# Performance work log

Hardware: AMD Instinct MI355X
Metric: run time of the kernel (lower is better)

## Reference

```python
import jax, jax.numpy as jnp
import numpy as np

B, H, SQ, SK, D, INT, F = 1, 32, 2048, 2048, 128, 128, 32
THOLD = 0.5


def _mlp(x, W1, b1, W2, b2, W3, b3):
    # x: [b,h,s,d]; W*: [h,out,in] (torch Linear layout), y = x @ W^T + b, per head
    h = jax.nn.silu(jnp.einsum('bhsd,hid->bhsi', x, W1) + b1[None, :, None, :])
    h = jax.nn.silu(jnp.einsum('bhsi,hji->bhsj', h, W2) + b2[None, :, None, :])
    return jnp.einsum('bhsj,hfj->bhsf', h, W3) + b3[None, :, None, :]


def setup_inputs() -> dict:
    key = jax.random.key(0)
    ks = jax.random.split(key, 16)
    sc = 0.05  # small init so tanh stays in its linear-ish range
    inp = {
        'K': jax.random.normal(ks[0], (B, H, SK, D), jnp.float32),
        'Q': jax.random.normal(ks[1], (B, H, SQ, D), jnp.float32),
        'Wk1': jax.random.normal(ks[2], (H, INT, D), jnp.float32) * sc,
        'bk1': jax.random.normal(ks[3], (H, INT), jnp.float32) * sc,
        'Wk2': jax.random.normal(ks[4], (H, INT, INT), jnp.float32) * sc,
        'bk2': jax.random.normal(ks[5], (H, INT), jnp.float32) * sc,
        'Wk3': jax.random.normal(ks[6], (H, F, INT), jnp.float32) * sc,
        'bk3': jax.random.normal(ks[7], (H, F), jnp.float32) * sc,
        'Wq1': jax.random.normal(ks[8], (H, INT, D), jnp.float32) * sc,
        'bq1': jax.random.normal(ks[9], (H, INT), jnp.float32) * sc,
        'Wq2': jax.random.normal(ks[10], (H, INT, INT), jnp.float32) * sc,
        'bq2': jax.random.normal(ks[11], (H, INT), jnp.float32) * sc,
        'Wq3': jax.random.normal(ks[12], (H, F, INT), jnp.float32) * sc,
        'bq3': jax.random.normal(ks[13], (H, F), jnp.float32) * sc,
    }
    return inp


def reference(K, Q, Wk1, bk1, Wk2, bk2, Wk3, bk3, Wq1, bq1, Wq2, bq2, Wq3, bq3):
    # soft (hard=False) path of USA.forward
    Kl = jnp.tanh(_mlp(K, Wk1, bk1, Wk2, bk2, Wk3, bk3))  # [b,h,sk,F]
    Ql = jnp.tanh(_mlp(Q, Wq1, bq1, Wq2, bq2, Wq3, bq3))  # [b,h,sq,F]
    scores = jnp.einsum('bhtf,bhsf->bhts', Ql, Kl)        # [b,h,sq,sk]
    sq, sk = Q.shape[2], K.shape[2]
    causal = jnp.tril(jnp.ones((sq, sk), dtype=bool), k=sk - sq)
    mask_val = jnp.asarray(jnp.finfo(scores.dtype).min, scores.dtype)
    scores = jnp.where(causal[None, None], scores, mask_val)
    return jax.nn.sigmoid(scores - THOLD)
```

## Files before the change

### kernel.cpp

```cpp
#include <hip/hip_runtime.h>

#define NH  32
#define SEQ 2048
#define DIM 128
#define FD  32

typedef short          short8 __attribute__((ext_vector_type(8)));
typedef float          f32x4  __attribute__((ext_vector_type(4)));
typedef unsigned short u16x8  __attribute__((ext_vector_type(8)));

static __device__ __forceinline__ unsigned short f2bf(float f) {
    unsigned int u = __builtin_bit_cast(unsigned int, f);
    u += 0x7fffu + ((u >> 16) & 1u);
    return (unsigned short)(u >> 16);
}
static __device__ __forceinline__ float fexp(float x) {
    return __builtin_amdgcn_exp2f(x * 1.44269504088896f);
}
static __device__ __forceinline__ float sigm(float x) {
    return __builtin_amdgcn_rcpf(1.0f + fexp(-x));
}
static __device__ __forceinline__ float silu_f(float x) { return x * sigm(x); }
static __device__ __forceinline__ float tanh_f(float x) {
    return 1.0f - 2.0f * __builtin_amdgcn_rcpf(fexp(2.0f * x) + 1.0f);
}

#define WPH 36864
#define WPS (32 * WPH)

__global__ __launch_bounds__(256) void prep_weights(
    const float* __restrict__ Wk1, const float* __restrict__ Wk2,
    const float* __restrict__ Wk3, const float* __restrict__ Wq1,
    const float* __restrict__ Wq2, const float* __restrict__ Wq3,
    unsigned short* __restrict__ wimg) {
    int c = blockIdx.x * 256 + threadIdx.x;
    int s = (c >= 147456) ? 1 : 0;
    c -= s * 147456;
    const float* src;
    int dst;
    int sB = s * WPS;
    if (c < 65536) {
        int h = c >> 11, idx = c & 2047;
        int r = idx >> 4, jb = (idx & 15) * 8;
        src = (s ? Wq1 : Wk1) + h * 16384 + r * 128 + jb;
        dst = sB + h * WPH + r * 128 + (jb ^ ((r & 7) << 3));
    } else if (c < 131072) {
        int cc = c - 65536;
        int h = cc >> 11, idx = cc & 2047;
        int r = idx >> 4, jb = (idx & 15) * 8;
        src = (s ? Wq2 : Wk2) + h * 16384 + r * 128 + jb;
        dst = sB + h * WPH + 16384 + r * 128 + (jb ^ ((r & 7) << 3));
    } else {
        int cc = c - 131072;
        int h = cc >> 9, idx = cc & 511;
        int r = idx >> 4, jb = (idx & 15) * 8;
        src = (s ? Wq3 : Wk3) + h * 4096 + r * 128 + jb;
        dst = sB + h * WPH + 32768 + r * 128 + (jb ^ ((r & 7) << 3));
    }
    f32x4 u0 = *(const f32x4*)src;
    f32x4 u1 = *(const f32x4*)(src + 4);
    u16x8 p;
    p[0] = f2bf(u0[0]); p[1] = f2bf(u0[1]); p[2] = f2bf(u0[2]); p[3] = f2bf(u0[3]);
    p[4] = f2bf(u1[0]); p[5] = f2bf(u1[1]); p[6] = f2bf(u1[2]); p[7] = f2bf(u1[3]);
    *(u16x8*)(&wimg[dst]) = p;
}

template <int OT, int ACT>
static __device__ __forceinline__ void compute_layer(
    const short8 a[4], const unsigned short* W,
    const float* __restrict__ bias, unsigned short* dst, int lane, int wid) {
    int r0 = lane & 15, q = lane >> 4, kb = q * 8;
#pragma unroll
    for (int ot = 0; ot < OT; ++ot) {
        int wrow = ot * 16 + r0;
        int sw   = (wrow & 7) << 3;
        short8 b[4];
#pragma unroll
        for (int ks = 0; ks < 4; ++ks)
            b[ks] = *(const short8*)(&W[wrow * 128 + ((ks * 32 + kb) ^ sw)]);
        f32x4 acc = {0.f, 0.f, 0.f, 0.f};
#pragma unroll
        for (int ks = 0; ks < 4; ++ks)
            acc = __builtin_amdgcn_mfma_f32_16x16x32_bf16(a[ks], b[ks], acc, 0, 0, 0);
        float bv = bias[wrow];
#pragma unroll
        for (int r = 0; r < 4; ++r) {
            float y = acc[r] + bv;
            float v = (ACT == 0) ? silu_f(y) : tanh_f(y);
            int orow = wid * 16 + q * 4 + r;
            int ocol = ot * 16 + r0;
            dst[orow * 128 + (ocol ^ ((orow & 7) << 3))] = f2bf(v);
        }
    }
}

static __device__ __forceinline__ void compute_layer3_reg(
    const short8 a[4], const short8 w3f[2][4],
    const float* __restrict__ bias, unsigned short* dst, int lane, int wid) {
    int r0 = lane & 15, q = lane >> 4;
#pragma unroll
    for (int ot = 0; ot < 2; ++ot) {
        f32x4 acc = {0.f, 0.f, 0.f, 0.f};
#pragma unroll
        for (int ks = 0; ks < 4; ++ks)
            acc = __builtin_amdgcn_mfma_f32_16x16x32_bf16(a[ks], w3f[ot][ks], acc, 0, 0, 0);
        float bv = bias[ot * 16 + r0];
#pragma unroll
        for (int r = 0; r < 4; ++r) {
            float v = tanh_f(acc[r] + bv);
            dst[(wid * 16 + q * 4 + r) * FD + ot * 16 + r0] = f2bf(v);
        }
    }
}

__global__ __launch_bounds__(256) void mlp_kernel(
    const float* __restrict__ K,  const float* __restrict__ Q,
    const float* __restrict__ bk1, const float* __restrict__ bk2,
    const float* __restrict__ bk3, const float* __restrict__ bq1,
    const float* __restrict__ bq2, const float* __restrict__ bq3,
    const unsigned short* __restrict__ wimg,
    unsigned short* __restrict__ Kl, unsigned short* __restrict__ Ql) {
    __shared__ unsigned short wb[128 * 128];
    __shared__ unsigned short act[64 * 128];
    __shared__ unsigned short outb[64 * FD];
    int raw = blockIdx.x;
    int bid = (raw & 7) * 256 + (raw >> 3);
    int tb  = bid & 31;
    int h   = (bid >> 5) & 31;
    int s   = bid >> 10;

    const float* X  = s ? Q : K;
    const unsigned short* Wb = wimg + s * WPS + h * WPH;
    const float* B1 = (s ? bq1 : bk1) + h * 128;
    const float* B2 = (s ? bq2 : bk2) + h * 128;
    const float* B3 = (s ? bq3 : bk3) + h * FD;
    unsigned short* gout = (s ? Ql : Kl) + ((size_t)h * SEQ + (size_t)tb * 64) * FD;

    int tid = threadIdx.x, lane = tid & 63, wid = tid >> 6;
    int r0 = lane & 15, kb = (lane >> 4) * 8;

    short8 w3f[2][4];
    {
        const unsigned short* W3g = Wb + 32768;
        int sw = (r0 & 7) << 3;
#pragma unroll
        for (int ot = 0; ot < 2; ++ot)
#pragma unroll
            for (int ks = 0; ks < 4; ++ks)
                w3f[ot][ks] = *(const short8*)(&W3g[(ot * 16 + r0) * 128 + ((ks * 32 + kb) ^ sw)]);
    }

    const u16x8* wsrc = (const u16x8*)Wb;
#pragma unroll
    for (int i = 0; i < 8; ++i)
        *(u16x8*)(&wb[(i * 256 + tid) * 8]) = wsrc[i * 256 + tid];

    short8 a[4];
    const float* xs = X + ((size_t)h * SEQ + (size_t)tb * 64) * DIM;
    int row = wid * 16 + r0;
#pragma unroll
    for (int ks = 0; ks < 4; ++ks) {
        const float* p = xs + row * 128 + ks * 32 + kb;
        f32x4 u0 = *(const f32x4*)p;
        f32x4 u1 = *(const f32x4*)(p + 4);
        short8 t;
        t[0] = f2bf(u0[0]); t[1] = f2bf(u0[1]); t[2] = f2bf(u0[2]); t[3] = f2bf(u0[3]);
        t[4] = f2bf(u1[0]); t[5] = f2bf(u1[1]); t[6] = f2bf(u1[2]); t[7] = f2bf(u1[3]);
        a[ks] = t;
    }
    __syncthreads();
    compute_layer<8, 0>(a, wb, B1, act, lane, wid);
    __syncthreads();
#pragma unroll
    for (int i = 0; i < 8; ++i)
        *(u16x8*)(&wb[(i * 256 + tid) * 8]) = wsrc[2048 + i * 256 + tid];
    __syncthreads();
    {
        int sw = (row & 7) << 3;
#pragma unroll
        for (int ks = 0; ks < 4; ++ks)
            a[ks] = *(const short8*)(&act[row * 128 + ((ks * 32 + kb) ^ sw)]);
    }
    compute_layer<8, 0>(a, wb, B2, act, lane, wid);
    {
        int sw = (row & 7) << 3;
#pragma unroll
        for (int ks = 0; ks < 4; ++ks)
            a[ks] = *(const short8*)(&act[row * 128 + ((ks * 32 + kb) ^ sw)]);
    }
    compute_layer3_reg(a, w3f, B3, outb, lane, wid);
    __syncthreads();
    *(u16x8*)(gout + tid * 8) = *(const u16x8*)(&outb[tid * 8]);
}

__global__ __launch_bounds__(256) void score_kernel(
    const unsigned short* __restrict__ Ql, const unsigned short* __restrict__ Kl,
    float* __restrict__ out) {
    int bid = blockIdx.x;
    int h   = bid >> 8;
    int tr  = (bid >> 4) & 15;
    int tc  = bid & 15;
    int tq0 = tr * 128, tk0 = tc * 128;
    int tid = threadIdx.x;
    float* ob = out + (size_t)h * SEQ * SEQ;

    if (tc > tr) {
        f32x4 z = {0.f, 0.f, 0.f, 0.f};
        for (int it = 0; it < 16; ++it) {
            int row = tq0 + it * 8 + (tid >> 5);
            int c0  = tk0 + (tid & 31) * 4;
            *(f32x4*)(ob + (size_t)row * SEQ + c0) = z;
        }
        return;
    }
    bool diag = (tc == tr);
    __shared__ float sb[2][16 * 130];
    int lane = tid & 63;
    int wid  = tid >> 6;
    int r0   = lane & 15;
    int kb   = (lane >> 4) * 8;

    short8 aq[8], bk[2];
#pragma unroll
    for (int i = 0; i < 8; ++i)
        aq[i] = *(const short8*)(Ql + ((size_t)h * SEQ + tq0 + i * 16 + r0) * FD + kb);
#pragma unroll
    for (int ct = 0; ct < 2; ++ct)
        bk[ct] = *(const short8*)(Kl + ((size_t)h * SEQ + tk0 + wid * 32 + ct * 16 + r0) * FD + kb);

#pragma unroll
    for (int p = 0; p < 8; ++p) {
        float* my = sb[p & 1];
#pragma unroll
        for (int ct = 0; ct < 2; ++ct) {
            f32x4 acc = {0.f, 0.f, 0.f, 0.f};
            acc = __builtin_amdgcn_mfma_f32_16x16x32_bf16(aq[p], bk[ct], acc, 0, 0, 0);
#pragma unroll
            for (int r = 0; r < 4; ++r) {
                int lr  = (lane >> 4) * 4 + r;
                int col = wid * 32 + ct * 16 + r0;
                float o = sigm(acc[r] - 0.5f);
                if (diag && (tk0 + col) > (tq0 + p * 16 + lr)) o = 0.0f;
                my[lr * 130 + col] = o;
            }
        }
        __syncthreads();
#pragma unroll
        for (int j = 0; j < 2; ++j) {
            int row = (tid >> 5) + j * 8;
            int c0  = (tid & 31) * 4;
            f32x4 v = *(const f32x4*)(&my[row * 130 + c0]);
            *(f32x4*)(ob + (size_t)(tq0 + p * 16 + row) * SEQ + tk0 + c0) = v;
        }
    }
}

extern "C" void kernel_launch(void* const* d_in, const int* in_sizes, int n_in,
                              void* d_out, int out_size, void* d_ws, size_t ws_size,
                              hipStream_t stream) {
    const float* K   = (const float*)d_in[0];
    const float* Q   = (const float*)d_in[1];
    const float* Wk1 = (const float*)d_in[2];
    const float* bk1 = (const float*)d_in[3];
    const float* Wk2 = (const float*)d_in[4];
    const float* bk2 = (const float*)d_in[5];
    const float* Wk3 = (const float*)d_in[6];
    const float* bk3 = (const float*)d_in[7];
    const float* Wq1 = (const float*)d_in[8];
    const float* bq1 = (const float*)d_in[9];
    const float* Wq2 = (const float*)d_in[10];
    const float* bq2 = (const float*)d_in[11];
    const float* Wq3 = (const float*)d_in[12];
    const float* bq3 = (const float*)d_in[13];

    unsigned short* Kl   = (unsigned short*)d_ws;
    unsigned short* Ql   = Kl + (size_t)NH * SEQ * FD;
    unsigned short* wimg = Ql + (size_t)NH * SEQ * FD;

    prep_weights<<<dim3(1152), dim3(256), 0, stream>>>(
        Wk1, Wk2, Wk3, Wq1, Wq2, Wq3, wimg);

    mlp_kernel<<<dim3(2 * NH * (SEQ / 64)), dim3(256), 0, stream>>>(
        K, Q, bk1, bk2, bk3, bq1, bq2, bq3, wimg, Kl, Ql);

    score_kernel<<<dim3(NH * 16 * 16), dim3(256), 0, stream>>>(
        Ql, Kl, (float*)d_out);
}
```

Measured before the change: 139.9 us.

## Retile score kernel to 64x512 tiles with XCD-aware block remap

The score kernel's output tiles change from 128x128 to 64x512, so each wave covers 128 key columns and each output row is written as one full 2 KB contiguous segment. Block indices are remapped with a stride-8 swizzle, presumably to spread heads across XCDs. The double-buffered LDS staging becomes a single 16x516 buffer guarded by two raw barriers per pass. The intent is wider coalesced stores for this write-bound kernel. The cost is more masked work on the diagonal, since any 512-wide tile crossing the diagonal now computes sigmoid for columns that end up zeroed.

After: 141.0 us. No clear change (+0.8%).

```diff
diff --git a/kernel.cpp b/kernel.cpp
--- a/kernel.cpp
+++ b/kernel.cpp
@@ -196,62 +196,72 @@
 __global__ __launch_bounds__(256) void score_kernel(
     const unsigned short* __restrict__ Ql, const unsigned short* __restrict__ Kl,
     float* __restrict__ out) {
-    int bid = blockIdx.x;
-    int h   = bid >> 8;
-    int tr  = (bid >> 4) & 15;
-    int tc  = bid & 15;
-    int tq0 = tr * 128, tk0 = tc * 128;
+    int raw = blockIdx.x;
+    int bid = (raw & 7) * 512 + (raw >> 3);
+    int h   = bid >> 7;
+    int i   = (bid >> 2) & 31;
+    int j   = bid & 3;
+    int tq0 = i * 64, tk0 = j * 512;
     int tid = threadIdx.x;
     float* ob = out + (size_t)h * SEQ * SEQ;
 
-    if (tc > tr) {
+    if (tk0 > tq0 + 63) {
         f32x4 z = {0.f, 0.f, 0.f, 0.f};
-        for (int it = 0; it < 16; ++it) {
+#pragma unroll
+        for (int it = 0; it < 8; ++it) {
             int row = tq0 + it * 8 + (tid >> 5);
-            int c0  = tk0 + (tid & 31) * 4;
-            *(f32x4*)(ob + (size_t)row * SEQ + c0) = z;
+            float* dst = ob + (size_t)row * SEQ + tk0 + (tid & 31) * 4;
+#pragma unroll
+            for (int rep = 0; rep < 4; ++rep)
+                *(f32x4*)(dst + rep * 128) = z;
         }
         return;
     }
-    bool diag = (tc == tr);
-    __shared__ float sb[2][16 * 130];
+    bool diag = (tk0 + 511 > tq0);
+    __shared__ float sb[16 * 516];
     int lane = tid & 63;
-    int wid  = tid >> 6;
+    int w    = tid >> 6;
     int r0   = lane & 15;
-    int kb   = (lane >> 4) * 8;
-
-    short8 aq[8], bk[2];
-#pragma unroll
-    for (int i = 0; i < 8; ++i)
-        aq[i] = *(const short8*)(Ql + ((size_t)h * SEQ + tq0 + i * 16 + r0) * FD + kb);
-#pragma unroll
-    for (int ct = 0; ct < 2; ++ct)
-        bk[ct] = *(const short8*)(Kl + ((size_t)h * SEQ + tk0 + wid * 32 + ct * 16 + r0) * FD + kb);
-
-#pragma unroll
-    for (int p = 0; p < 8; ++p) {
-        float* my = sb[p & 1];
-#pragma unroll
-        for (int ct = 0; ct < 2; ++ct) {
+    int q    = lane >> 4;
+    int kb   = q * 8;
+
+    short8 aq[4], bk[8];
+#pragma unroll
+    for (int p = 0; p < 4; ++p)
+        aq[p] = *(const short8*)(Ql + ((size_t)h * SEQ + tq0 + p * 16 + r0) * FD + kb);
+#pragma unroll
+    for (int ct = 0; ct < 8; ++ct)
+        bk[ct] = *(const short8*)(Kl + ((size_t)h * SEQ + tk0 + w * 128 + ct * 16 + r0) * FD + kb);
+
+#pragma unroll
+    for (int p = 0; p < 4; ++p) {
+#pragma unroll
+        for (int ct = 0; ct < 8; ++ct) {
             f32x4 acc = {0.f, 0.f, 0.f, 0.f};
             acc = __builtin_amdgcn_mfma_f32_16x16x32_bf16(aq[p], bk[ct], acc, 0, 0, 0);
+            int colw = w * 128 + ct * 16 + r0;
 #pragma unroll
             for (int r = 0; r < 4; ++r) {
-                int lr  = (lane >> 4) * 4 + r;
-                int col = wid * 32 + ct * 16 + r0;
+                int lr = q * 4 + r;
                 float o = sigm(acc[r] - 0.5f);
-                if (diag && (tk0 + col) > (tq0 + p * 16 + lr)) o = 0.0f;
-                my[lr * 130 + col] = o;
+                if (diag && (tk0 + colw) > (tq0 + p * 16 + lr)) o = 0.0f;
+                sb[lr * 516 + colw] = o;
             }
         }
-        __syncthreads();
-#pragma unroll
-        for (int j = 0; j < 2; ++j) {
-            int row = (tid >> 5) + j * 8;
-            int c0  = (tid & 31) * 4;
-            f32x4 v = *(const f32x4*)(&my[row * 130 + c0]);
-            *(f32x4*)(ob + (size_t)(tq0 + p * 16 + row) * SEQ + tk0 + c0) = v;
-        }
+        asm volatile("s_waitcnt lgkmcnt(0)" ::: "memory");
+        __builtin_amdgcn_s_barrier();
+#pragma unroll
+        for (int rr = 0; rr < 4; ++rr) {
+            int srow = w * 4 + rr;
+            const float* src = &sb[srow * 516];
+            float* dst = ob + (size_t)(tq0 + p * 16 + srow) * SEQ + tk0;
+#pragma unroll
+            for (int rep = 0; rep < 2; ++rep) {
+                f32x4 v = *(const f32x4*)(src + lane * 4 + rep * 256);
+                *(f32x4*)(dst + lane * 4 + rep * 256) = v;
+            }
+        }
+        __builtin_amdgcn_s_barrier();
     }
 }
 
@@ -283,6 +293,6 @@
     mlp_kernel<<<dim3(2 * NH * (SEQ / 64)), dim3(256), 0, stream>>>(
         K, Q, bk1, bk2, bk3, bq1, bq2, bq3, wimg, Kl, Ql);
 
-    score_kernel<<<dim3(NH * 16 * 16), dim3(256), 0, stream>>>(
+    score_kernel<<<dim3(NH * 32 * 4), dim3(256), 0, stream>>>(
         Ql, Kl, (float*)d_out);
 }
```
